# Performance work log

Hardware: AMD Instinct MI355X
Metric: run time of the kernel (lower is better)

Reference implementation:

```python
import jax, jax.numpy as jnp
import numpy as np

N, S, E, D = 20000, 4096, 640000, 256
SPARSITY = 0.02  # fraction of nonzero entries in the normalized matrix


def setup_inputs() -> dict:
    key = jax.random.key(0)
    ks = jax.random.split(key, 6)
    u = jax.random.uniform(ks[0], (N, S), dtype=jnp.float32)
    init = jnp.where(u < SPARSITY, u, 0.0)
    edge_index = jax.random.randint(ks[1], (2, E), 0, N, dtype=jnp.int32)
    edge_attr = jax.random.uniform(ks[2], (E,), dtype=jnp.float32)
    # Projection MLP params (Linear(1,16) -> ReLU -> Linear(16,D))
    w1 = jax.random.normal(ks[3], (1, 16), dtype=jnp.float32)
    b1 = jnp.zeros((16,), dtype=jnp.float32)
    w2 = jax.random.normal(ks[4], (16, D), dtype=jnp.float32) / np.float32(np.sqrt(16))
    b2 = jnp.zeros((D,), dtype=jnp.float32)
    # GCN weight (xavier-ish)
    W = jax.random.normal(ks[5], (D, D), dtype=jnp.float32) / np.float32(np.sqrt(D))
    return {"init": init, "edge_index": edge_index, "edge_attr": edge_attr,
            "w1": w1, "b1": b1, "w2": w2, "b2": b2, "W": W}


def reference(init, edge_index, edge_attr, w1, b1, w2, b2, W):
    n, s = init.shape
    # Projection: torch code feeds the nonzero COLUMN INDICES (as floats) of each
    # row through the MLP and means them. Vectorized: precompute MLP(j) for all
    # column indices j, then do a masked mean via a single matmul.
    idx = jnp.arange(s, dtype=init.dtype)[:, None]          # [S,1]
    phi = jax.nn.relu(idx @ w1 + b1) @ w2 + b2              # [S,D]
    mask = (init != 0).astype(init.dtype)                   # [N,S]
    cnt = mask.sum(axis=1)                                  # [N]
    # rows with zero nonzeros yield zero embedding (matches torch branch)
    h = (mask @ phi) / jnp.maximum(cnt, 1.0)[:, None]       # [N,D]

    # 3-layer GCN: scatter_add of h[row]*attr into col, then mm + relu
    row, col = edge_index[0], edge_index[1]
    for _ in range(3):
        h_agg = jax.ops.segment_sum(h[row] * edge_attr[:, None], col,
                                    num_segments=n)          # [N,D]
        h = jax.nn.relu(h_agg @ W)
    return h
```

## Files before the change

kernel.cpp:

```cpp
#include <hip/hip_runtime.h>


#define N_NODES 20000
#define S_COLS  4096
#define E_EDGES 640000
#define D_DIM   256

typedef unsigned short bf16_t;
typedef __attribute__((ext_vector_type(8))) short short8;
typedef __attribute__((ext_vector_type(4))) float f32x4;

__device__ __forceinline__ float bf2f(bf16_t u) {
    union { unsigned int i; float f; } v; v.i = ((unsigned int)u) << 16; return v.f;
}
__device__ __forceinline__ bf16_t f2bf(float x) {
    union { float f; unsigned int i; } v; v.f = x;
    unsigned int r = v.i + 0x7FFF + ((v.i >> 16) & 1);
    return (bf16_t)(r >> 16);
}
__device__ __forceinline__ float lo_bf(unsigned int u) {
    union { unsigned int i; float f; } v; v.i = u << 16; return v.f;
}
__device__ __forceinline__ float hi_bf(unsigned int u) {
    union { unsigned int i; float f; } v; v.i = u & 0xFFFF0000u; return v.f;
}
__device__ __forceinline__ unsigned int pack_bf(float a, float b) {
    return (unsigned int)f2bf(a) | ((unsigned int)f2bf(b) << 16);
}

__global__ void __launch_bounds__(256, 4)
mega_kernel(const float* __restrict__ init_m,
            const float* __restrict__ w1, const float* __restrict__ b1,
            const float* __restrict__ w2, const float* __restrict__ b2,
            bf16_t* __restrict__ h,
            const int* __restrict__ eidx, int* __restrict__ cnt,
            const float* __restrict__ W,
            bf16_t* __restrict__ Wt_hi, bf16_t* __restrict__ Wt_lo) {
    int b = blockIdx.x;
    int t = threadIdx.x;

    if (b >= 5000) {
        int bb = b - 5000;
        if (bb < 2500) {
            int e = bb * 256 + t;
            atomicAdd(&cnt[eidx[E_EDGES + e]], 1);
        } else {
            int k = bb - 2500;
            float w = W[k * D_DIM + t];
            bf16_t hi = f2bf(w);
            bf16_t lo = f2bf(w - bf2f(hi));
            Wt_hi[t * D_DIM + k] = hi;
            Wt_lo[t * D_DIM + k] = lo;
        }
        return;
    }

    __shared__ float w2s[16][256];
#pragma unroll
    for (int k = 0; k < 16; ++k) w2s[k][t] = w2[k * D_DIM + t];
    __syncthreads();

    int wave = t >> 6, lane = t & 63;
    int row  = b * 4 + wave;

    float lw1[16], lb1[16];
#pragma unroll
    for (int k = 0; k < 16; ++k) { lw1[k] = w1[k]; lb1[k] = b1[k]; }

    const float4* rowp = (const float4*)(init_m + (size_t)row * S_COLS);
    float f[16] = {};
    float cn = 0.f;

#define PROC_COMP(val, jb)                                            \
    if ((val) != 0.f) {                                               \
        float jf = (float)(jb);                                       \
        _Pragma("unroll")                                             \
        for (int k = 0; k < 16; ++k)                                  \
            f[k] += fmaxf(jf * lw1[k] + lb1[k], 0.f);                 \
        cn += 1.f;                                                    \
    }

#pragma unroll 4
    for (int v = 0; v < 16; ++v) {
        float4 x = rowp[v * 64 + lane];
        int jb = (v * 64 + lane) * 4;
        PROC_COMP(x.x, jb)
        PROC_COMP(x.y, jb + 1)
        PROC_COMP(x.z, jb + 2)
        PROC_COMP(x.w, jb + 3)
    }
#undef PROC_COMP

#pragma unroll
    for (int off = 32; off > 0; off >>= 1) {
#pragma unroll
        for (int k = 0; k < 16; ++k) f[k] += __shfl_xor(f[k], off, 64);
        cn += __shfl_xor(cn, off, 64);
    }

    float4 b2v = *(const float4*)(b2 + 4 * lane);
    float o0 = cn * b2v.x, o1 = cn * b2v.y, o2 = cn * b2v.z, o3 = cn * b2v.w;
#pragma unroll
    for (int k = 0; k < 16; ++k) {
        float4 wv = *(const float4*)(&w2s[k][4 * lane]);
        o0 += f[k] * wv.x;  o1 += f[k] * wv.y;
        o2 += f[k] * wv.z;  o3 += f[k] * wv.w;
    }
    float inv = 1.f / fmaxf(cn, 1.f);
    uint2 o;
    o.x = pack_bf(o0 * inv, o1 * inv);
    o.y = pack_bf(o2 * inv, o3 * inv);
    *(uint2*)(h + (size_t)row * D_DIM + 4 * lane) = o;
}

__global__ void scan_kernel(const int* __restrict__ cnt, int* __restrict__ offs,
                            int* __restrict__ cur) {
    __shared__ int sdata[1024];
    int t = threadIdx.x;
    int base = t * 20;
    int vals[20];
    int local = 0;
#pragma unroll
    for (int k = 0; k < 20; ++k) {
        int idx = base + k;
        int v = (idx < N_NODES) ? cnt[idx] : 0;
        vals[k] = local;
        local += v;
    }
    sdata[t] = local;
    __syncthreads();
    for (int off = 1; off < 1024; off <<= 1) {
        int v = (t >= off) ? sdata[t - off] : 0;
        __syncthreads();
        sdata[t] += v;
        __syncthreads();
    }
    int prefix = (t == 0) ? 0 : sdata[t - 1];
#pragma unroll
    for (int k = 0; k < 20; ++k) {
        int idx = base + k;
        if (idx < N_NODES) {
            int o = prefix + vals[k];
            offs[idx] = o;
            cur[idx]  = o;
        }
    }
    if (t == 1023) offs[N_NODES] = sdata[1023];
}

__global__ void fill_kernel(const int* __restrict__ eidx, const float* __restrict__ attr,
                            int* __restrict__ cur, int* __restrict__ src_s,
                            float* __restrict__ attr_s) {
    int e = blockIdx.x * 256 + threadIdx.x;
    if (e < E_EDGES) {
        int r = eidx[e];
        int c = eidx[E_EDGES + e];
        int pos = atomicAdd(&cur[c], 1);
        src_s[pos]  = r;
        attr_s[pos] = attr[e];
    }
}

__global__ void gather_kernel(const bf16_t* __restrict__ h,
                              const int* __restrict__ offs,
                              const int* __restrict__ src_s,
                              const float* __restrict__ attr_s,
                              bf16_t* __restrict__ g) {
    int wid  = (blockIdx.x * blockDim.x + threadIdx.x) >> 6;
    int lane = threadIdx.x & 63;
    if (wid >= N_NODES) return;
    int half = lane >> 5;
    int l32  = lane & 31;
    int e0 = offs[wid], e1 = offs[wid + 1];

    float acc[8] = {};
    for (int base = e0; base < e1; base += 64) {
        int n = e1 - base; if (n > 64) n = 64;
        int   r_l = 0; float a_l = 0.f;
        if (lane < n) { r_l = src_s[base + lane]; a_l = attr_s[base + lane]; }
        int nn = (n + 15) & ~15;
        for (int q = 0; q < nn; q += 16) {
#pragma unroll
            for (int u = 0; u < 8; ++u) {
                int   sl = q + 2 * u + half;
                int   r  = __shfl(r_l, sl, 64);
                float a  = __shfl(a_l, sl, 64);
                uint4 v  = ((const uint4*)(h + (size_t)r * D_DIM))[l32];
                acc[0] += lo_bf(v.x) * a;  acc[1] += hi_bf(v.x) * a;
                acc[2] += lo_bf(v.y) * a;  acc[3] += hi_bf(v.y) * a;
                acc[4] += lo_bf(v.z) * a;  acc[5] += hi_bf(v.z) * a;
                acc[6] += lo_bf(v.w) * a;  acc[7] += hi_bf(v.w) * a;
            }
        }
    }
#pragma unroll
    for (int i = 0; i < 8; ++i) acc[i] += __shfl_xor(acc[i], 32, 64);

    if (half == 0) {
        uint4 o;
        o.x = pack_bf(acc[0], acc[1]);
        o.y = pack_bf(acc[2], acc[3]);
        o.z = pack_bf(acc[4], acc[5]);
        o.w = pack_bf(acc[6], acc[7]);
        ((uint4*)(g + (size_t)wid * D_DIM))[l32] = o;
    }
}

__global__ void gemm_relu_kernel(const bf16_t* __restrict__ g,
                                 const bf16_t* __restrict__ Wt_hi,
                                 const bf16_t* __restrict__ Wt_lo,
                                 bf16_t* __restrict__ hdst, float* __restrict__ fdst) {
    __shared__ bf16_t Bs[2][256][64];
    int tid  = threadIdx.x;
    int w    = tid >> 6;
    int lane = tid & 63;
    int quad = lane >> 4;
    int id16 = lane & 15;
    int bm   = blockIdx.x * 64 + w * 16;

    const bf16_t* arow = g + (size_t)(bm + id16) * D_DIM;
    short8 areg[8];
#pragma unroll
    for (int i = 0; i < 8; ++i)
        areg[i] = *(const short8*)(arow + i * 32 + quad * 8);

    f32x4 acc[16];
#pragma unroll
    for (int nt = 0; nt < 16; ++nt) acc[nt] = (f32x4){0.f, 0.f, 0.f, 0.f};

    char* bs = (char*)Bs;
    int seg = tid & 7;

    {
        const bf16_t* src = Wt_hi;
#pragma unroll
        for (int pp = 0; pp < 8; ++pp) {
            int n = (tid >> 3) + pp * 32;
            unsigned off = (unsigned)(n * 128 + seg * 16) ^ (unsigned)((n & 7) << 4);
            *(uint4*)(bs + off) = *(const uint4*)(src + (size_t)n * D_DIM + seg * 8);
        }
    }
    __syncthreads();

    for (int c = 0; c < 8; ++c) {
        int buf = c & 1;
        if (c < 7) {
            int cn = c + 1;
            const bf16_t* src = (cn < 4) ? Wt_hi : Wt_lo;
            int ks = (cn & 3) * 64;
            unsigned bofs = (unsigned)((buf ^ 1) * 32768);
#pragma unroll
            for (int pp = 0; pp < 8; ++pp) {
                int n = (tid >> 3) + pp * 32;
                unsigned off = bofs + ((unsigned)(n * 128 + seg * 16) ^ (unsigned)((n & 7) << 4));
                *(uint4*)(bs + off) = *(const uint4*)(src + (size_t)n * D_DIM + ks + seg * 8);
            }
        }
        unsigned bofs = (unsigned)(buf * 32768);
#pragma unroll
        for (int kk2 = 0; kk2 < 2; ++kk2) {
            short8 a = areg[(c & 3) * 2 + kk2];
            unsigned kbyte = (unsigned)(kk2 * 64 + quad * 16);
#pragma unroll
            for (int nt = 0; nt < 16; ++nt) {
                int n = nt * 16 + id16;
                unsigned off = bofs + (((unsigned)(n * 128) + kbyte) ^ (unsigned)((n & 7) << 4));
                short8 bfr = *(const short8*)(bs + off);
                acc[nt] = __builtin_amdgcn_mfma_f32_16x16x32_bf16(a, bfr, acc[nt], 0, 0, 0);
            }
        }
        __syncthreads();
    }

#pragma unroll
    for (int nt = 0; nt < 16; ++nt) {
#pragma unroll
        for (int r = 0; r < 4; ++r) {
            int m = bm + quad * 4 + r;
            if (m < N_NODES) {
                float v = fmaxf(acc[nt][r], 0.f);
                int n = nt * 16 + id16;
                if (hdst) hdst[(size_t)m * D_DIM + n] = f2bf(v);
                else      fdst[(size_t)m * D_DIM + n] = v;
            }
        }
    }
}

extern "C" void kernel_launch(void* const* d_in, const int* in_sizes, int n_in,
                              void* d_out, int out_size, void* d_ws, size_t ws_size,
                              hipStream_t stream) {
    const float* init_m = (const float*)d_in[0];
    const int*   eidx   = (const int*)  d_in[1];
    const float* attr   = (const float*)d_in[2];
    const float* w1     = (const float*)d_in[3];
    const float* b1     = (const float*)d_in[4];
    const float* w2     = (const float*)d_in[5];
    const float* b2     = (const float*)d_in[6];
    const float* Wm     = (const float*)d_in[7];
    float* out = (float*)d_out;

    char* ws = (char*)d_ws;
    bf16_t* hbuf   = (bf16_t*)ws;
    bf16_t* gbuf   = (bf16_t*)(ws + 10240000);
    int*    cnt    = (int*)   (ws + 20529152);
    int*    offs   = (int*)   (ws + 20609152);
    int*    cur    = (int*)   (ws + 20689408);
    int*    src_s  = (int*)   (ws + 20769408);
    float*  attr_s = (float*) (ws + 23329408);
    bf16_t* Wt_hi  = (bf16_t*)(ws + 25889408);
    bf16_t* Wt_lo  = (bf16_t*)(ws + 26020480);

    hipMemsetAsync(ws + 20480000, 0, 129152, stream);

    mega_kernel<<<5000 + 2500 + 256, 256, 0, stream>>>(
        init_m, w1, b1, w2, b2, hbuf, eidx, cnt, Wm, Wt_hi, Wt_lo);
    scan_kernel<<<1, 1024, 0, stream>>>(cnt, offs, cur);
    fill_kernel<<<(E_EDGES + 255) / 256, 256, 0, stream>>>(eidx, attr, cur, src_s, attr_s);

    dim3 ggrid((N_NODES * 64 + 255) / 256);
    dim3 mgrid((N_NODES + 63) / 64);
    for (int it = 0; it < 3; ++it) {
        gather_kernel<<<ggrid, 256, 0, stream>>>(hbuf, offs, src_s, attr_s, gbuf);
        if (it == 2)
            gemm_relu_kernel<<<mgrid, 256, 0, stream>>>(gbuf, Wt_hi, Wt_lo,
                                                        (bf16_t*)nullptr, out);
        else
            gemm_relu_kernel<<<mgrid, 256, 0, stream>>>(gbuf, Wt_hi, Wt_lo,
                                                        hbuf, (float*)nullptr);
    }
}
```

Baseline: 781.8 us.

## Retile GEMM into 160x64 output blocks with a fully resident W slice and prefetched A

The GEMM+ReLU kernel now splits the output along N into four 64-column slices via a 2D grid. Each block loads its full hi/lo W slice into shared memory once and loops over ten 16-row M tiles, prefetching the next A tile into registers. This removes the per-chunk double-buffered W reloads and the repeated __syncthreads, and trades them for more blocks each re-reading A rows and a 64KB LDS footprint per block. The old row bounds check is dropped, which relies on 125*160 equalling N exactly.

```diff
diff --git a/kernel.cpp b/kernel.cpp
--- a/kernel.cpp
+++ b/kernel.cpp
@@ -206,84 +206,90 @@
     }
 }
 
-__global__ void gemm_relu_kernel(const bf16_t* __restrict__ g,
-                                 const bf16_t* __restrict__ Wt_hi,
-                                 const bf16_t* __restrict__ Wt_lo,
-                                 bf16_t* __restrict__ hdst, float* __restrict__ fdst) {
-    __shared__ bf16_t Bs[2][256][64];
+__global__ void __launch_bounds__(256, 2)
+gemm_relu_kernel(const bf16_t* __restrict__ g,
+                 const bf16_t* __restrict__ Wt_hi,
+                 const bf16_t* __restrict__ Wt_lo,
+                 bf16_t* __restrict__ hdst, float* __restrict__ fdst) {
+    __shared__ bf16_t Bs[64][512];
     int tid  = threadIdx.x;
     int w    = tid >> 6;
     int lane = tid & 63;
     int quad = lane >> 4;
     int id16 = lane & 15;
-    int bm   = blockIdx.x * 64 + w * 16;
-
-    const bf16_t* arow = g + (size_t)(bm + id16) * D_DIM;
+    int bn   = blockIdx.y * 64;
+    int bm0  = blockIdx.x * 160;
+
+    char* bs = (char*)Bs;
+
+    {
+        int tn0 = tid >> 4;
+        int ts0 = tid & 15;
+#pragma unroll
+        for (int it = 0; it < 16; ++it) {
+            int n   = tn0 + (it & 3) * 16;
+            int seg = ts0 + (it >> 2) * 16;
+            const bf16_t* src = (seg < 32 ? Wt_hi : Wt_lo)
+                              + (size_t)(bn + n) * D_DIM + (seg & 31) * 8;
+            unsigned off = (unsigned)(n * 1024 + seg * 16) ^ (unsigned)((n & 7) << 4);
+            *(uint4*)(bs + off) = *(const uint4*)src;
+        }
+    }
+
+    int r0 = bm0 + w * 16;
+    const bf16_t* arow = g + (size_t)(r0 + id16) * D_DIM;
     short8 areg[8];
 #pragma unroll
     for (int i = 0; i < 8; ++i)
         areg[i] = *(const short8*)(arow + i * 32 + quad * 8);
 
-    f32x4 acc[16];
-#pragma unroll
-    for (int nt = 0; nt < 16; ++nt) acc[nt] = (f32x4){0.f, 0.f, 0.f, 0.f};
-
-    char* bs = (char*)Bs;
-    int seg = tid & 7;
-
-    {
-        const bf16_t* src = Wt_hi;
-#pragma unroll
-        for (int pp = 0; pp < 8; ++pp) {
-            int n = (tid >> 3) + pp * 32;
-            unsigned off = (unsigned)(n * 128 + seg * 16) ^ (unsigned)((n & 7) << 4);
-            *(uint4*)(bs + off) = *(const uint4*)(src + (size_t)n * D_DIM + seg * 8);
-        }
-    }
     __syncthreads();
 
-    for (int c = 0; c < 8; ++c) {
-        int buf = c & 1;
-        if (c < 7) {
-            int cn = c + 1;
-            const bf16_t* src = (cn < 4) ? Wt_hi : Wt_lo;
-            int ks = (cn & 3) * 64;
-            unsigned bofs = (unsigned)((buf ^ 1) * 32768);
-#pragma unroll
-            for (int pp = 0; pp < 8; ++pp) {
-                int n = (tid >> 3) + pp * 32;
-                unsigned off = bofs + ((unsigned)(n * 128 + seg * 16) ^ (unsigned)((n & 7) << 4));
-                *(uint4*)(bs + off) = *(const uint4*)(src + (size_t)n * D_DIM + ks + seg * 8);
+    unsigned swz   = (unsigned)((id16 & 7) << 4);
+    unsigned nbase = (unsigned)(id16 * 1024);
+
+    for (int t = w; t < 10; t += 4) {
+        short8 anext[8];
+        int tn = t + 4;
+        if (tn < 10) {
+            const bf16_t* an = g + (size_t)(bm0 + tn * 16 + id16) * D_DIM;
+#pragma unroll
+            for (int i = 0; i < 8; ++i)
+                anext[i] = *(const short8*)(an + i * 32 + quad * 8);
+        }
+
+        f32x4 acc[4];
+#pragma unroll
+        for (int nt = 0; nt < 4; ++nt) acc[nt] = (f32x4){0.f, 0.f, 0.f, 0.f};
+
+#pragma unroll
+        for (int ks = 0; ks < 8; ++ks) {
+            short8 a = areg[ks];
+            unsigned kb = ((unsigned)(ks * 64 + quad * 16)) ^ swz;
+#pragma unroll
+            for (int nt = 0; nt < 4; ++nt) {
+                unsigned off = (unsigned)(nt * 16384) + nbase + kb;
+                short8 bh = *(const short8*)(bs + off);
+                short8 bl = *(const short8*)(bs + off + 512);
+                acc[nt] = __builtin_amdgcn_mfma_f32_16x16x32_bf16(a, bh, acc[nt], 0, 0, 0);
+                acc[nt] = __builtin_amdgcn_mfma_f32_16x16x32_bf16(a, bl, acc[nt], 0, 0, 0);
             }
         }
-        unsigned bofs = (unsigned)(buf * 32768);
-#pragma unroll
-        for (int kk2 = 0; kk2 < 2; ++kk2) {
-            short8 a = areg[(c & 3) * 2 + kk2];
-            unsigned kbyte = (unsigned)(kk2 * 64 + quad * 16);
-#pragma unroll
-            for (int nt = 0; nt < 16; ++nt) {
-                int n = nt * 16 + id16;
-                unsigned off = bofs + (((unsigned)(n * 128) + kbyte) ^ (unsigned)((n & 7) << 4));
-                short8 bfr = *(const short8*)(bs + off);
-                acc[nt] = __builtin_amdgcn_mfma_f32_16x16x32_bf16(a, bfr, acc[nt], 0, 0, 0);
-            }
-        }
-        __syncthreads();
-    }
-
-#pragma unroll
-    for (int nt = 0; nt < 16; ++nt) {
-#pragma unroll
-        for (int r = 0; r < 4; ++r) {
-            int m = bm + quad * 4 + r;
-            if (m < N_NODES) {
+
+        int mrow = bm0 + t * 16;
+#pragma unroll
+        for (int nt = 0; nt < 4; ++nt) {
+#pragma unroll
+            for (int r = 0; r < 4; ++r) {
+                int m = mrow + quad * 4 + r;
+                int n = bn + nt * 16 + id16;
                 float v = fmaxf(acc[nt][r], 0.f);
-                int n = nt * 16 + id16;
                 if (hdst) hdst[(size_t)m * D_DIM + n] = f2bf(v);
                 else      fdst[(size_t)m * D_DIM + n] = v;
             }
         }
+#pragma unroll
+        for (int i = 0; i < 8; ++i) areg[i] = anext[i];
     }
 }
 
@@ -319,7 +325,7 @@
     fill_kernel<<<(E_EDGES + 255) / 256, 256, 0, stream>>>(eidx, attr, cur, src_s, attr_s);
 
     dim3 ggrid((N_NODES * 64 + 255) / 256);
-    dim3 mgrid((N_NODES + 63) / 64);
+    dim3 mgrid(125, 4);
     for (int it = 0; it < 3; ++it) {
         gather_kernel<<<ggrid, 256, 0, stream>>>(hbuf, offs, src_s, attr_s, gbuf);
         if (it == 2)
```

Result: faster. 761.5 us (-2.6%).
